# Performance work log

Measured on AMD Instinct MI355X. Metric: run time of the kernel, lower is better.

Reference implementation:

```python
import jax, jax.numpy as jnp
import numpy as np

N = 100000   # nodes
E = 3200000  # edges (avg degree 32)
IN, H, OUT = 128, 256, 40
EPS = 1e-5


def _glorot(key, fan_in, fan_out):
    s = jnp.sqrt(2.0 / (fan_in + fan_out))
    return jax.random.normal(key, (fan_in, fan_out), jnp.float32) * s


def setup_inputs() -> dict:
    key = jax.random.key(0)
    ks = jax.random.split(key, 6)
    edge_index = jax.random.randint(ks[0], (2, E), 0, N, dtype=jnp.int64)
    z = jax.random.normal(ks[1], (N, IN), jnp.float32) * 0.1
    return {
        "edge_index": edge_index,
        "z": z,
        "W1": _glorot(ks[2], IN, H), "b1": jnp.zeros((H,), jnp.float32),
        "g1": jnp.ones((H,), jnp.float32), "beta1": jnp.zeros((H,), jnp.float32),
        "W2": _glorot(ks[3], H, H), "b2": jnp.zeros((H,), jnp.float32),
        "g2": jnp.ones((H,), jnp.float32), "beta2": jnp.zeros((H,), jnp.float32),
        "W3": _glorot(ks[4], H, OUT), "b3": jnp.zeros((OUT,), jnp.float32),
    }


def _gcn_norm(edge_index):
    # add self-loops, compute symmetric normalization D^-1/2 (A+I) D^-1/2
    loops = jnp.arange(N, dtype=edge_index.dtype)
    src = jnp.concatenate([edge_index[0], loops])
    dst = jnp.concatenate([edge_index[1], loops])
    deg = jax.ops.segment_sum(jnp.ones_like(dst, jnp.float32), dst, num_segments=N)
    dinv = jnp.where(deg > 0, jax.lax.rsqrt(deg), 0.0)
    norm = dinv[src] * dinv[dst]  # [E+N]
    return src, dst, norm


def _conv(x, W, b, src, dst, norm):
    h = x @ W                              # [N, F_out]
    msg = h[src] * norm[:, None]           # gather + scale, [E+N, F_out]
    return jax.ops.segment_sum(msg, dst, num_segments=N) + b


def _bn(x, g, beta):
    m = x.mean(axis=0)
    v = x.var(axis=0)  # biased variance (training-mode BatchNorm)
    return (x - m) * jax.lax.rsqrt(v + EPS) * g + beta


def reference(edge_index, z, W1, b1, g1, beta1, W2, b2, g2, beta2, W3, b3):
    src, dst, norm = _gcn_norm(edge_index)
    x = jax.nn.relu(_bn(_conv(z, W1, b1, src, dst, norm), g1, beta1))
    x = jax.nn.relu(_bn(_conv(x, W2, b2, src, dst, norm), g2, beta2))
    return _conv(x, W3, b3, src, dst, norm)  # [N, OUT]
```

## Files before the change

kernel.cpp:

```cpp
#include <hip/hip_runtime.h>


#define NN   100000
#define NE   3200000
#define FIN  128
#define FH   256
#define FOUT 40
#define EPSV 1e-5f

#define BSH   7
#define NBKT  ((NN + 127) >> BSH)
#define CAPB  8192
#define CHNK  4096

typedef __attribute__((ext_vector_type(8))) short bf8;
typedef __attribute__((ext_vector_type(4))) float f32x4;

__device__ __forceinline__ unsigned short f2bf(float x) {
    unsigned int u = __float_as_uint(x);
    unsigned int r = u + 0x7fffu + ((u >> 16) & 1u);
    return (unsigned short)(r >> 16);
}
__device__ __forceinline__ float bf2f(unsigned short h) {
    return __uint_as_float(((unsigned int)h) << 16);
// ... 101 lines not shown
    __syncthreads();
    for (int i = tid; i < tot; i += 256) {
        unsigned int v = st[i];
        atomicAdd(&lcnt[v >> 17], 1);
    }
    __syncthreads();
    int pi = 0;
    if (tid < 128) lscan[0][tid] = lcnt[tid];
    __syncthreads();
    for (int off = 1; off < 128; off <<= 1) {
        if (tid < 128) {
            int x = lscan[pi][tid];
            if (tid >= off) x += lscan[pi][tid - off];
            lscan[pi ^ 1][tid] = x;
        }
        __syncthreads();
        pi ^= 1;
    }
    if (tid < 128) {
        int c = lcnt[tid];
        int excl = lscan[pi][tid] - c;
        lcur[tid] = excl;
        int node = (b << BSH) + tid;
        if (node < NN) {
            cntg[node] = c;
            dinv[node] = rsqrtf((float)(c + 1));
            rowptr[node] = bb + excl;
        }
    }
    __syncthreads();
    for (int i = tid; i < tot; i += 256) {
        unsigned int v = st[i];
        int pos = atomicAdd(&lcur[v >> 17], 1);
        csr[bb + pos] = (int)(v & 0x1ffffu);
    }
}

__global__ void k_wprep(const float* __restrict__ W1, unsigned short* __restrict__ W1h,
                        unsigned short* __restrict__ W1l,
                        const float* __restrict__ W2, unsigned short* __restrict__ W2h,
                        unsigned short* __restrict__ W2l,
                        const float* __restrict__ W3, unsigned short* __restrict__ W3h,
                        unsigned short* __restrict__ W3l) {
    int idx = blockIdx.x * blockDim.x + threadIdx.x;
    const float* W;
    unsigned short *Wh, *Wl;
    int K, M, MP;
    if (idx < 256 * 128) {
        W = W1; Wh = W1h; Wl = W1l; K = 128; M = 256; MP = 256;
    } else if (idx < 256 * 128 + 256 * 256) {
        idx -= 256 * 128;
        W = W2; Wh = W2h; Wl = W2l; K = 256; M = 256; MP = 256;
    } else if (idx < 256 * 128 + 256 * 256 + 64 * 256) {
        idx -= 256 * 128 + 256 * 256;
        W = W3; Wh = W3h; Wl = W3l; K = 256; M = 40; MP = 64;
    } else {
        return;
    }
    int m = idx / K, k = idx - m * K;
    float v = (m < M) ? W[(size_t)k * M + m] : 0.f;
    unsigned short h, l;
    f2bf2(v, h, l);
    size_t dst = ((size_t)(k >> 5) * MP + m) * 32 + (k & 31);
    Wh[dst] = h;
    Wl[dst] = l;
}

__global__ __launch_bounds__(256) void k_zpb8(const float* __restrict__ z,
                                              const float* __restrict__ dinv,
                                              unsigned char* __restrict__ zp8,
                                              float* __restrict__ scaleZ) {
    int wv = (blockIdx.x * blockDim.x + threadIdx.x) >> 6;
    int lane = threadIdx.x & 63;
    if (wv >= NN) return;
    float2 v = *(const float2*)(z + (size_t)wv * FIN + lane * 2);
    float d = dinv[wv];
    float a0 = v.x * d, a1 = v.y * d;
    float m = fmaxf(fabsf(a0), fabsf(a1));
#pragma unroll
    for (int off = 1; off < 64; off <<= 1) m = fmaxf(m, __shfl_xor(m, off));
    float inv = m > 0.f ? 127.f / m : 0.f;
    int q0 = (int)rintf(a0 * inv), q1 = (int)rintf(a1 * inv);
    unsigned short pk = (unsigned short)((q0 & 0xff) | ((q1 & 0xff) << 8));
    *(unsigned short*)(zp8 + (size_t)wv * FIN + lane * 2) = pk;
    if (lane == 0) scaleZ[wv] = m * (1.f / 127.f);
}

__global__ __launch_bounds__(256) void k_bnr8(const unsigned short* __restrict__ x,
                                              const float* __restrict__ scale,
                                              const float* __restrict__ shift,
                                              const float* __restrict__ dinv,
                                              unsigned char* __restrict__ y8,
                                              float* __restrict__ scaleY) {
    int wv = (blockIdx.x * blockDim.x + threadIdx.x) >> 6;
    int lane = threadIdx.x & 63;
    if (wv >= NN) return;
    uint2 u = *(const uint2*)(x + (size_t)wv * 256 + lane * 4);
    float4 sc = *(const float4*)(scale + lane * 4);
    float4 sh = *(const float4*)(shift + lane * 4);
    float d = dinv[wv];
    float v0 = fmaxf(__uint_as_float(u.x << 16) * sc.x + sh.x, 0.f) * d;
    float v1 = fmaxf(__uint_as_float(u.x & 0xffff0000u) * sc.y + sh.y, 0.f) * d;
    float v2 = fmaxf(__uint_as_float(u.y << 16) * sc.z + sh.z, 0.f) * d;
    float v3 = fmaxf(__uint_as_float(u.y & 0xffff0000u) * sc.w + sh.w, 0.f) * d;
    float m = fmaxf(fmaxf(v0, v1), fmaxf(v2, v3));
#pragma unroll
    for (int off = 1; off < 64; off <<= 1) m = fmaxf(m, __shfl_xor(m, off));
    float inv = m > 0.f ? 255.f / m : 0.f;
    unsigned int q0 = (unsigned int)(v0 * inv + 0.5f);
    unsigned int q1 = (unsigned int)(v1 * inv + 0.5f);
    unsigned int q2 = (unsigned int)(v2 * inv + 0.5f);
    unsigned int q3 = (unsigned int)(v3 * inv + 0.5f);
    *(unsigned int*)(y8 + (size_t)wv * 256 + lane * 4) = q0 | (q1 << 8) | (q2 << 16) | (q3 << 24);
    if (lane == 0) scaleY[wv] = m * (1.f / 255.f);
}

template <int F, bool SIGNED>
__global__ __launch_bounds__(256) void k_agg8(const unsigned char* __restrict__ tab,
                                              const float* __restrict__ rscale,
                                              const float* __restrict__ dinv,
                                              const int* __restrict__ rowptr,
                                              const int* __restrict__ cnt,
                                              const int* __restrict__ csr,
                                              unsigned short* __restrict__ oa) {
    const int wid = threadIdx.x >> 6;
    const int lane = threadIdx.x & 63;
    const int wstep = (blockDim.x >> 6) * gridDim.x;
    constexpr int B = F / 64;
    const int off = lane * B;
    for (int row0 = blockIdx.x * (blockDim.x >> 6) + wid; row0 < NN; row0 += wstep) {
        const int row = __builtin_amdgcn_readfirstlane(row0);
        const int rp = __builtin_amdgcn_readfirstlane(rowptr[row]);
        const int cn = __builtin_amdgcn_readfirstlane(cnt[row]);
        float acc[B];
        {
            float s = rscale[row];
            if constexpr (B == 4) {
                unsigned int u = *(const unsigned int*)(tab + (size_t)row * F + off);
                acc[0] = s * ub(u, 0); acc[1] = s * ub(u, 1);
                acc[2] = s * ub(u, 2); acc[3] = s * ub(u, 3);
            } else {
                unsigned int u = *(const unsigned short*)(tab + (size_t)row * F + off);
                acc[0] = s * sbyte(u, 0); acc[1] = s * sbyte(u, 1);
            }
        }
        int e = 0;
        for (; e + 8 <= cn; e += 8) {
            int idx[8];
            float s[8];
            unsigned int u[8];
#pragma unroll
            for (int j = 0; j < 8; j++) idx[j] = csr[rp + e + j];
#pragma unroll
            for (int j = 0; j < 8; j++) s[j] = rscale[idx[j]];
#pragma unroll
            for (int j = 0; j < 8; j++) {
                if constexpr (B == 4)
                    u[j] = *(const unsigned int*)(tab + (size_t)idx[j] * F + off);
                else
                    u[j] = *(const unsigned short*)(tab + (size_t)idx[j] * F + off);
            }
#pragma unroll
            for (int j = 0; j < 8; j++) {
                if constexpr (B == 4) {
                    acc[0] += s[j] * ub(u[j], 0); acc[1] += s[j] * ub(u[j], 1);
                    acc[2] += s[j] * ub(u[j], 2); acc[3] += s[j] * ub(u[j], 3);
                } else {
                    acc[0] += s[j] * sbyte(u[j], 0); acc[1] += s[j] * sbyte(u[j], 1);
                }
            }
        }
        for (; e < cn; e++) {
            int idx = csr[rp + e];
            float s = rscale[idx];
            if constexpr (B == 4) {
                unsigned int u = *(const unsigned int*)(tab + (size_t)idx * F + off);
                acc[0] += s * ub(u, 0); acc[1] += s * ub(u, 1);
                acc[2] += s * ub(u, 2); acc[3] += s * ub(u, 3);
            } else {
                unsigned int u = *(const unsigned short*)(tab + (size_t)idx * F + off);
                acc[0] += s * sbyte(u, 0); acc[1] += s * sbyte(u, 1);
            }
        }
        float d = dinv[row];
        size_t p = (size_t)row * F + off;
        if constexpr (B == 4) {
            uint2 o;
            o.x = (unsigned int)f2bf(acc[0] * d) | ((unsigned int)f2bf(acc[1] * d) << 16);
            o.y = (unsigned int)f2bf(acc[2] * d) | ((unsigned int)f2bf(acc[3] * d) << 16);
            *(uint2*)(oa + p) = o;
        } else {
            *(unsigned int*)(oa + p) =
                (unsigned int)f2bf(acc[0] * d) | ((unsigned int)f2bf(acc[1] * d) << 16);
        }
    }
}

template <int K>
__global__ __launch_bounds__(256) void k_gemm(const unsigned short* __restrict__ A,
                                              const unsigned short* __restrict__ Wth,
                                              const unsigned short* __restrict__ Wtl,
                                              const float* __restrict__ bias,
                                              unsigned short* __restrict__ outX,
                                              float* __restrict__ s1,
                                              float* __restrict__ s2) {
    __shared__ unsigned short sA[64][40];
    const int t = threadIdx.x;
    const int w = t >> 6, lane = t & 63;
    const int quad = lane >> 4, l16 = lane & 15;
    const int rowBase = blockIdx.y * 64;
    const int colW = blockIdx.x * 128 + w * 32;
    f32x4 acc[4][2];
#pragma unroll
    for (int i = 0; i < 4; i++)
#pragma unroll
        for (int j = 0; j < 2; j++) acc[i][j] = (f32x4)0.f;

    for (int k0 = 0; k0 < K; k0 += 32) {
        int gr = rowBase + (t >> 2);
        int4 v = {0, 0, 0, 0};
        if (gr < NN) v = *(const int4*)(A + (size_t)gr * K + k0 + (t & 3) * 8);
        __syncthreads();
        *(int4*)&sA[t >> 2][(t & 3) * 8] = v;
        __syncthreads();
        const int kb = k0 >> 5;
        bf8 bh[2], bl[2];
#pragma unroll
        for (int j = 0; j < 2; j++) {
            size_t bo = ((size_t)(kb * 256 + colW + j * 16 + l16)) * 32 + quad * 8;
            bh[j] = *(const bf8*)(Wth + bo);
            bl[j] = *(const bf8*)(Wtl + bo);
        }
#pragma unroll
        for (int i = 0; i < 4; i++) {
            bf8 a = *(const bf8*)&sA[i * 16 + l16][quad * 8];
#pragma unroll
            for (int j = 0; j < 2; j++) {
                acc[i][j] = __builtin_amdgcn_mfma_f32_16x16x32_bf16(a, bh[j], acc[i][j], 0, 0, 0);
                acc[i][j] = __builtin_amdgcn_mfma_f32_16x16x32_bf16(a, bl[j], acc[i][j], 0, 0, 0);
            }
        }
    }
#pragma unroll
    for (int j = 0; j < 2; j++) {
        int col = colW + j * 16 + l16;
        float b = bias[col];
        float s1p = 0.f, s2p = 0.f;
#pragma unroll
        for (int i = 0; i < 4; i++) {
#pragma unroll
            for (int r = 0; r < 4; r++) {
                int row = rowBase + i * 16 + quad * 4 + r;
                if (row < NN) {
                    float v = acc[i][j][r] + b;
                    s1p += v;
                    s2p += v * v;
                    outX[(size_t)row * 256 + col] = f2bf(v);
                }
            }
        }
        s1p += __shfl_xor(s1p, 16); s1p += __shfl_xor(s1p, 32);
        s2p += __shfl_xor(s2p, 16); s2p += __shfl_xor(s2p, 32);
        if (quad == 0) {
            atomicAdd(&s1[col], s1p);
            atomicAdd(&s2[col], s2p);
        }
    }
}

__global__ __launch_bounds__(256) void k_mgemm3(const unsigned short* __restrict__ y2,
                                                const unsigned short* __restrict__ Wth,
                                                const unsigned short* __restrict__ Wtl,
                                                unsigned char* __restrict__ H8,
                                                float* __restrict__ scaleH) {
    __shared__ unsigned short sA[128][40];
    __shared__ float sM[128][4];
    const int t = threadIdx.x;
    const int w = t >> 6, lane = t & 63;
    const int quad = lane >> 4, l16 = lane & 15;
    const int rowBase = blockIdx.x << 7;
    f32x4 acc[8];
#pragma unroll
    for (int i = 0; i < 8; i++) acc[i] = (f32x4)0.f;

    for (int k0 = 0; k0 < 256; k0 += 32) {
        const int kb = k0 >> 5;
        int id0 = t, id1 = t + 256;
        int gr0 = rowBase + (id0 >> 2), gr1 = rowBase + (id1 >> 2);
        int4 zz = {0, 0, 0, 0};
        int4 v0 = (gr0 < NN) ? *(const int4*)(y2 + (size_t)gr0 * 256 + k0 + (id0 & 3) * 8) : zz;
        int4 v1 = (gr1 < NN) ? *(const int4*)(y2 + (size_t)gr1 * 256 + k0 + (id1 & 3) * 8) : zz;
        __syncthreads();
        *(int4*)&sA[id0 >> 2][(id0 & 3) * 8] = v0;
        *(int4*)&sA[id1 >> 2][(id1 & 3) * 8] = v1;
        __syncthreads();
        size_t bo = ((size_t)(kb * 64 + w * 16 + l16)) * 32 + quad * 8;
        bf8 bh = *(const bf8*)(Wth + bo);
        bf8 bl = *(const bf8*)(Wtl + bo);
#pragma unroll
        for (int i = 0; i < 8; i++) {
            bf8 a = *(const bf8*)&sA[i * 16 + l16][quad * 8];
            acc[i] = __builtin_amdgcn_mfma_f32_16x16x32_bf16(a, bh, acc[i], 0, 0, 0);
            acc[i] = __builtin_amdgcn_mfma_f32_16x16x32_bf16(a, bl, acc[i], 0, 0, 0);
        }
    }
#pragma unroll
    for (int i = 0; i < 8; i++) {
#pragma unroll
        for (int r = 0; r < 4; r++) {
            float m = fabsf(acc[i][r]);
            m = fmaxf(m, __shfl_xor(m, 1));
            m = fmaxf(m, __shfl_xor(m, 2));
            m = fmaxf(m, __shfl_xor(m, 4));
            m = fmaxf(m, __shfl_xor(m, 8));
            if (l16 == 0) sM[i * 16 + quad * 4 + r][w] = m;
        }
    }
    __syncthreads();
    const int col = w * 16 + l16;
#pragma unroll
    for (int i = 0; i < 8; i++) {
#pragma unroll
        for (int r = 0; r < 4; r++) {
            int rloc = i * 16 + quad * 4 + r;
            int row = rowBase + rloc;
            float m = fmaxf(fmaxf(sM[rloc][0], sM[rloc][1]), fmaxf(sM[rloc][2], sM[rloc][3]));
            float inv = m > 0.f ? 127.f / m : 0.f;
            if (row < NN) {
                int q = (int)rintf(acc[i][r] * inv);
                H8[(size_t)row * 64 + col] = (unsigned char)(q & 0xff);
                if (w == 0 && l16 == 0) scaleH[row] = m * (1.f / 127.f);
            }
        }
    }
}

__global__ __launch_bounds__(256) void k_aggfb8(const unsigned char* __restrict__ tab,
                                                const float* __restrict__ rscale,
                                                const float* __restrict__ dinv,
                                                const int* __restrict__ rowptr,
                                                const int* __restrict__ cnt,
                                                const int* __restrict__ csr,
                                                const float* __restrict__ bias,
                                                float* __restrict__ out) {
    const int wid = threadIdx.x >> 6;
    const int lane = threadIdx.x & 63;
    const int wstep = (blockDim.x >> 6) * gridDim.x;
    for (int row0 = blockIdx.x * (blockDim.x >> 6) + wid; row0 < NN; row0 += wstep) {
        const int row = __builtin_amdgcn_readfirstlane(row0);
        const int rp = __builtin_amdgcn_readfirstlane(rowptr[row]);
        const int cn = __builtin_amdgcn_readfirstlane(cnt[row]);
        float acc = rscale[row] * (float)(int)(signed char)tab[(size_t)row * 64 + lane];
        int e = 0;
        for (; e + 8 <= cn; e += 8) {
            int idx[8];
            float s[8];
            float v[8];
#pragma unroll
            for (int j = 0; j < 8; j++) idx[j] = csr[rp + e + j];
#pragma unroll
            for (int j = 0; j < 8; j++) s[j] = rscale[idx[j]];
#pragma unroll
            for (int j = 0; j < 8; j++)
                v[j] = (float)(int)(signed char)tab[(size_t)idx[j] * 64 + lane];
#pragma unroll
            for (int j = 0; j < 8; j++) acc += s[j] * v[j];
        }
        for (; e < cn; e++) {
            int idx = csr[rp + e];
            float s = rscale[idx];
            acc += s * (float)(int)(signed char)tab[(size_t)idx * 64 + lane];
        }
        if (lane < FOUT) out[(size_t)row * FOUT + lane] = acc * dinv[row] + bias[lane];
    }
}

__global__ void k_bnfold(const float* __restrict__ s1, const float* __restrict__ s2,
                         const float* __restrict__ g, const float* __restrict__ be,
                         float* __restrict__ scale, float* __restrict__ shift) {
    int c = threadIdx.x;
    if (c < 256) {
        float mean = s1[c] * (1.f / NN);
        float var = s2[c] * (1.f / NN) - mean * mean;
        float sc = g[c] * rsqrtf(var + EPSV);
        scale[c] = sc;
        shift[c] = be[c] - mean * sc;
    }
}

__global__ void k_bnr(const unsigned short* __restrict__ x,
                      const float* __restrict__ scale, const float* __restrict__ shift,
                      const float* __restrict__ dinv, unsigned short* __restrict__ oy) {
    int i = blockIdx.x * blockDim.x + threadIdx.x;
    if (i >= NN * 128) return;
    int row = i >> 7;
    int c = (i & 127) * 2;
    unsigned int u = ((const unsigned int*)x)[i];
    float x0 = __uint_as_float(u << 16);
    float x1 = __uint_as_float(u & 0xffff0000u);
    float d = dinv[row];
    float v0 = fmaxf(x0 * scale[c + 0] + shift[c + 0], 0.f) * d;
    float v1 = fmaxf(x1 * scale[c + 1] + shift[c + 1], 0.f) * d;
    ((unsigned int*)oy)[i] = (unsigned int)f2bf(v0) | ((unsigned int)f2bf(v1) << 16);
}

extern "C" void kernel_launch(void* const* d_in, const int* in_sizes, int n_in,
                              void* d_out, int out_size, void* d_ws, size_t ws_size,
                              hipStream_t stream) {
    const int* ei = (const int*)d_in[0];
    const float* z = (const float*)d_in[1];
    const float* W1 = (const float*)d_in[2];
    const float* b1 = (const float*)d_in[3];
    const float* g1 = (const float*)d_in[4];
    const float* be1 = (const float*)d_in[5];
    const float* W2 = (const float*)d_in[6];
    const float* b2 = (const float*)d_in[7];
    const float* g2 = (const float*)d_in[8];
    const float* be2 = (const float*)d_in[9];
    const float* W3 = (const float*)d_in[10];
    const float* b3 = (const float*)d_in[11];
    float* out = (float*)d_out;

    char* w = (char*)d_ws;
    size_t o = 0;
    auto take = [&](size_t bytes) {
        char* p = w + o;
        o = (o + bytes + 255) & ~(size_t)255;
        return p;
    };
    int* cnt = (int*)take((size_t)NN * 4);
    int* rowptr = (int*)take((size_t)NN * 4);
    int* gcur = (int*)take(NBKT * 4);
    int* bbase = (int*)take(NBKT * 4);
    int* csr = (int*)take((size_t)NE * 4);
    unsigned int* staging = (unsigned int*)take((size_t)NBKT * CAPB * 4);
    float* dinv = (float*)take((size_t)NN * 4);
    float* stat = (float*)take(4 * 256 * 4);
    float* sc1 = (float*)take(256 * 4);
    float* sh1 = (float*)take(256 * 4);
    float* sc2 = (float*)take(256 * 4);
    float* sh2 = (float*)take(256 * 4);
    unsigned short* Wt1h = (unsigned short*)take(256 * 128 * 2);
    unsigned short* Wt1l = (unsigned short*)take(256 * 128 * 2);
    unsigned short* Wt2h = (unsigned short*)take(256 * 256 * 2);
    unsigned short* Wt2l = (unsigned short*)take(256 * 256 * 2);
    unsigned short* Wt3h = (unsigned short*)take(64 * 256 * 2);
    unsigned short* Wt3l = (unsigned short*)take(64 * 256 * 2);
    unsigned char* zp8 = (unsigned char*)take((size_t)NN * FIN);
    unsigned char* y1_8 = (unsigned char*)take((size_t)NN * FH);
    unsigned char* H8 = (unsigned char*)take((size_t)NN * 64);
    float* scaleZ = (float*)take((size_t)NN * 4);
    float* scaleY = (float*)take((size_t)NN * 4);
    float* scaleH = (float*)take((size_t)NN * 4);
    unsigned short* P1 = (unsigned short*)take((size_t)NN * 256 * 2);
    unsigned short* P2 = (unsigned short*)take((size_t)NN * 512 * 2);

    unsigned short* a1 = P1;
    unsigned short* x1 = P2;
    unsigned short* a2 = P2 + (size_t)NN * 256;
    unsigned short* x2 = P1;
    unsigned short* y2 = P2;
    float* s1a = stat, *s2a = stat + 256, *s1b = stat + 512, *s2b = stat + 768;

    hipMemsetAsync(gcur, 0, NBKT * 4, stream);
    hipMemsetAsync(stat, 0, 4 * 256 * 4, stream);

    k_bin<<<(NE + CHNK - 1) / CHNK, 256, 0, stream>>>(ei, gcur, staging);
    k_bucketscan<<<1, 256, 0, stream>>>(gcur, bbase);
    k_build<<<NBKT, 256, 0, stream>>>(staging, gcur, bbase, cnt, dinv, rowptr, csr);

    k_wprep<<<(256 * 128 + 256 * 256 + 64 * 256 + 255) / 256, 256, 0, stream>>>(
        W1, Wt1h, Wt1l, W2, Wt2h, Wt2l, W3, Wt3h, Wt3l);

    const int GR = (NN + 63) / 64;
    const int WV = (NN + 3) / 4;

    k_zpb8<<<WV, 256, 0, stream>>>(z, dinv, zp8, scaleZ);
    k_agg8<128, true><<<2560, 256, 0, stream>>>(zp8, scaleZ, dinv, rowptr, cnt, csr, a1);
    k_gemm<128><<<dim3(2, GR), 256, 0, stream>>>(a1, Wt1h, Wt1l, b1, x1, s1a, s2a);
    k_bnfold<<<1, 256, 0, stream>>>(s1a, s2a, g1, be1, sc1, sh1);
    k_bnr8<<<WV, 256, 0, stream>>>(x1, sc1, sh1, dinv, y1_8, scaleY);

    k_agg8<256, false><<<2560, 256, 0, stream>>>(y1_8, scaleY, dinv, rowptr, cnt, csr, a2);
    k_gemm<256><<<dim3(2, GR), 256, 0, stream>>>(a2, Wt2h, Wt2l, b2, x2, s1b, s2b);
    k_bnfold<<<1, 256, 0, stream>>>(s1b, s2b, g2, be2, sc2, sh2);
    k_bnr<<<(NN * 128 + 255) / 256, 256, 0, stream>>>(x2, sc2, sh2, dinv, y2);

    k_mgemm3<<<NBKT, 256, 0, stream>>>(y2, Wt3h, Wt3l, H8, scaleH);
    k_aggfb8<<<2560, 256, 0, stream>>>(H8, scaleH, dinv, rowptr, cnt, csr, b3, out);
}
```

Measured before the change: 815.8 us.

## Gather 16-byte chunks per lane across multiple edges in int8 aggregation

Restructures the int8 SpMM aggregation so each lane loads a 16-byte uint4 chunk of a neighbor row, with the wavefront split into groups that process several edges at once. Column indices and scales are loaded cooperatively, one per lane, then broadcast with shuffles. Partial sums are combined with xor-shuffle reductions and a select network before the bf16 store. The aim is fewer, wider memory transactions and more edges in flight per wave, at the cost of 16 accumulators per lane and extra shuffle and reduction work.

```diff
diff --git a/kernel.cpp b/kernel.cpp
--- a/kernel.cpp
+++ b/kernel.cpp
@@ -251,72 +251,111 @@
     const int wid = threadIdx.x >> 6;
     const int lane = threadIdx.x & 63;
     const int wstep = (blockDim.x >> 6) * gridDim.x;
-    constexpr int B = F / 64;
-    const int off = lane * B;
+    constexpr int G = 1024 / F;
+    constexpr int LPE = 64 / G;
+    constexpr int NS = 16 / G;
+    const int sub = lane & (LPE - 1);
+    const int grp = lane / LPE;
+    const size_t choff = (size_t)sub * 16;
     for (int row0 = blockIdx.x * (blockDim.x >> 6) + wid; row0 < NN; row0 += wstep) {
         const int row = __builtin_amdgcn_readfirstlane(row0);
         const int rp = __builtin_amdgcn_readfirstlane(rowptr[row]);
         const int cn = __builtin_amdgcn_readfirstlane(cnt[row]);
-        float acc[B];
+        float acc[16];
         {
-            float s = rscale[row];
-            if constexpr (B == 4) {
-                unsigned int u = *(const unsigned int*)(tab + (size_t)row * F + off);
-                acc[0] = s * ub(u, 0); acc[1] = s * ub(u, 1);
-                acc[2] = s * ub(u, 2); acc[3] = s * ub(u, 3);
-            } else {
-                unsigned int u = *(const unsigned short*)(tab + (size_t)row * F + off);
-                acc[0] = s * sbyte(u, 0); acc[1] = s * sbyte(u, 1);
-            }
-        }
-        int e = 0;
-        for (; e + 8 <= cn; e += 8) {
-            int idx[8];
-            float s[8];
-            unsigned int u[8];
-#pragma unroll
-            for (int j = 0; j < 8; j++) idx[j] = csr[rp + e + j];
-#pragma unroll
-            for (int j = 0; j < 8; j++) s[j] = rscale[idx[j]];
-#pragma unroll
-            for (int j = 0; j < 8; j++) {
-                if constexpr (B == 4)
-                    u[j] = *(const unsigned int*)(tab + (size_t)idx[j] * F + off);
-                else
-                    u[j] = *(const unsigned short*)(tab + (size_t)idx[j] * F + off);
-            }
-#pragma unroll
-            for (int j = 0; j < 8; j++) {
-                if constexpr (B == 4) {
-                    acc[0] += s[j] * ub(u[j], 0); acc[1] += s[j] * ub(u[j], 1);
-                    acc[2] += s[j] * ub(u[j], 2); acc[3] += s[j] * ub(u[j], 3);
-                } else {
-                    acc[0] += s[j] * sbyte(u[j], 0); acc[1] += s[j] * sbyte(u[j], 1);
+            float s0 = rscale[row];
+            float se = (grp == 0) ? s0 : 0.f;
+            uint4 u = *(const uint4*)(tab + (size_t)row * F + choff);
+            const unsigned int uw[4] = {u.x, u.y, u.z, u.w};
+#pragma unroll
+            for (int jw = 0; jw < 4; jw++)
+#pragma unroll
+                for (int jb = 0; jb < 4; jb++)
+                    acc[jw * 4 + jb] =
+                        se * (SIGNED ? sbyte(uw[jw], jb) : ub(uw[jw], jb));
+        }
+        for (int e = 0; e < cn; e += 64) {
+            const int rem = min(cn - e, 64);
+            int cv = row;
+            float sv = 0.f;
+            if (lane < rem) {
+                cv = csr[rp + e + lane];
+                sv = rscale[cv];
+            }
+            for (int q = 0; q < rem; q += 16) {
+                const int nslot = (min(rem - q, 16) + G - 1) / G;
+                int mi[NS];
+                float ms[NS];
+                uint4 u[NS];
+#pragma unroll
+                for (int t = 0; t < NS; t++) {
+                    if (t < nslot) {
+                        int srcl = q + t * G + grp;
+                        mi[t] = __shfl(cv, srcl);
+                        ms[t] = __shfl(sv, srcl);
+                    }
                 }
-            }
-        }
-        for (; e < cn; e++) {
-            int idx = csr[rp + e];
-            float s = rscale[idx];
-            if constexpr (B == 4) {
-                unsigned int u = *(const unsigned int*)(tab + (size_t)idx * F + off);
-                acc[0] += s * ub(u, 0); acc[1] += s * ub(u, 1);
-                acc[2] += s * ub(u, 2); acc[3] += s * ub(u, 3);
-            } else {
-                unsigned int u = *(const unsigned short*)(tab + (size_t)idx * F + off);
-                acc[0] += s * sbyte(u, 0); acc[1] += s * sbyte(u, 1);
-            }
-        }
-        float d = dinv[row];
-        size_t p = (size_t)row * F + off;
-        if constexpr (B == 4) {
+#pragma unroll
+                for (int t = 0; t < NS; t++) {
+                    if (t < nslot)
+                        u[t] = *(const uint4*)(tab + (size_t)mi[t] * F + choff);
+                }
+#pragma unroll
+                for (int t = 0; t < NS; t++) {
+                    if (t < nslot) {
+                        const unsigned int uw[4] = {u[t].x, u[t].y, u[t].z, u[t].w};
+#pragma unroll
+                        for (int jw = 0; jw < 4; jw++)
+#pragma unroll
+                            for (int jb = 0; jb < 4; jb++)
+                                acc[jw * 4 + jb] +=
+                                    ms[t] * (SIGNED ? sbyte(uw[jw], jb) : ub(uw[jw], jb));
+                    }
+                }
+            }
+        }
+        if constexpr (G == 4) {
+#pragma unroll
+            for (int j = 0; j < 16; j++) {
+                acc[j] += __shfl_xor(acc[j], 16);
+                acc[j] += __shfl_xor(acc[j], 32);
+            }
+        } else {
+#pragma unroll
+            for (int j = 0; j < 16; j++) {
+                acc[j] += __shfl_xor(acc[j], 8);
+                acc[j] += __shfl_xor(acc[j], 16);
+                acc[j] += __shfl_xor(acc[j], 32);
+            }
+        }
+        const float d = dinv[row];
+        if constexpr (G == 4) {
+            float av[4];
+#pragma unroll
+            for (int jj = 0; jj < 4; jj++) {
+                float a = (grp & 1) ? acc[4 + jj] : acc[jj];
+                float b = (grp & 1) ? acc[12 + jj] : acc[8 + jj];
+                av[jj] = (grp & 2) ? b : a;
+            }
             uint2 o;
-            o.x = (unsigned int)f2bf(acc[0] * d) | ((unsigned int)f2bf(acc[1] * d) << 16);
-            o.y = (unsigned int)f2bf(acc[2] * d) | ((unsigned int)f2bf(acc[3] * d) << 16);
-            *(uint2*)(oa + p) = o;
+            o.x = (unsigned int)f2bf(av[0] * d) | ((unsigned int)f2bf(av[1] * d) << 16);
+            o.y = (unsigned int)f2bf(av[2] * d) | ((unsigned int)f2bf(av[3] * d) << 16);
+            *(uint2*)(oa + (size_t)row * F + sub * 16 + grp * 4) = o;
         } else {
-            *(unsigned int*)(oa + p) =
-                (unsigned int)f2bf(acc[0] * d) | ((unsigned int)f2bf(acc[1] * d) << 16);
+            float av[2];
+#pragma unroll
+            for (int jj = 0; jj < 2; jj++) {
+                float x01 = (grp & 1) ? acc[2 + jj] : acc[0 + jj];
+                float x23 = (grp & 1) ? acc[6 + jj] : acc[4 + jj];
+                float x45 = (grp & 1) ? acc[10 + jj] : acc[8 + jj];
+                float x67 = (grp & 1) ? acc[14 + jj] : acc[12 + jj];
+                float y0 = (grp & 2) ? x23 : x01;
+                float y1 = (grp & 2) ? x67 : x45;
+                av[jj] = (grp & 4) ? y1 : y0;
+            }
+            unsigned int o =
+                (unsigned int)f2bf(av[0] * d) | ((unsigned int)f2bf(av[1] * d) << 16);
+            *(unsigned int*)(oa + (size_t)row * F + sub * 16 + grp * 2) = o;
         }
     }
 }
```

Measured after the change: 938.6 us. 15.0% more time.

## Slice quantized feature tables and aggregate 8 edges per wave in parallel

Applied to the files above, without the earlier changes.

The int8 feature tables written by the quantize kernels and the layer-3 GEMM are re-laid out as column slices of 32 or 64 bytes per node stored contiguously. Blocks are assigned to one slice, so the gather working set per kernel shrinks and is meant to stay resident in cache. Within a wave, 8 lane groups each fetch a different neighbor's slice row, the loads are software-pipelined, and the partial sums are reduced with cross-lane shuffles. The cost is more blocks walking the CSR (once per slice), extra shuffle reductions, and a small pad on the csr buffer to keep reads past the end in bounds.

```diff
diff --git a/kernel.cpp b/kernel.cpp
--- a/kernel.cpp
+++ b/kernel.cpp
@@ -207,7 +207,8 @@
     float inv = m > 0.f ? 127.f / m : 0.f;
     int q0 = (int)rintf(a0 * inv), q1 = (int)rintf(a1 * inv);
     unsigned short pk = (unsigned short)((q0 & 0xff) | ((q1 & 0xff) << 8));
-    *(unsigned short*)(zp8 + (size_t)wv * FIN + lane * 2) = pk;
+    *(unsigned short*)(zp8 + (size_t)(lane >> 4) * ((size_t)NN * 32) +
+                       (size_t)wv * 32 + ((lane * 2) & 31)) = pk;
     if (lane == 0) scaleZ[wv] = m * (1.f / 127.f);
 }
 
@@ -236,87 +237,120 @@
     unsigned int q1 = (unsigned int)(v1 * inv + 0.5f);
     unsigned int q2 = (unsigned int)(v2 * inv + 0.5f);
     unsigned int q3 = (unsigned int)(v3 * inv + 0.5f);
-    *(unsigned int*)(y8 + (size_t)wv * 256 + lane * 4) = q0 | (q1 << 8) | (q2 << 16) | (q3 << 24);
+    *(unsigned int*)(y8 + (size_t)(lane >> 4) * ((size_t)NN * 64) +
+                     (size_t)wv * 64 + ((lane * 4) & 63)) =
+        q0 | (q1 << 8) | (q2 << 16) | (q3 << 24);
     if (lane == 0) scaleY[wv] = m * (1.f / 255.f);
 }
 
-template <int F, bool SIGNED>
-__global__ __launch_bounds__(256) void k_agg8(const unsigned char* __restrict__ tab,
+template <int F, int SW, bool SIGNED>
+__global__ __launch_bounds__(256) void k_aggs(const unsigned char* __restrict__ tab,
                                               const float* __restrict__ rscale,
                                               const float* __restrict__ dinv,
                                               const int* __restrict__ rowptr,
                                               const int* __restrict__ cnt,
                                               const int* __restrict__ csr,
                                               unsigned short* __restrict__ oa) {
+    constexpr int NSL = F / SW;
+    constexpr int PB = SW / 8;
+    const int slice = blockIdx.x % NSL;
+    const int sb = blockIdx.x / NSL;
+    const int nsb = gridDim.x / NSL;
     const int wid = threadIdx.x >> 6;
     const int lane = threadIdx.x & 63;
-    const int wstep = (blockDim.x >> 6) * gridDim.x;
-    constexpr int B = F / 64;
-    const int off = lane * B;
-    for (int row0 = blockIdx.x * (blockDim.x >> 6) + wid; row0 < NN; row0 += wstep) {
+    const int g = lane >> 3;
+    const int fb = (lane & 7) * PB;
+    const unsigned char* tsl = tab + (size_t)slice * ((size_t)NN * SW);
+
+    for (int row0 = sb * 4 + wid; row0 < NN; row0 += nsb * 4) {
         const int row = __builtin_amdgcn_readfirstlane(row0);
         const int rp = __builtin_amdgcn_readfirstlane(rowptr[row]);
         const int cn = __builtin_amdgcn_readfirstlane(cnt[row]);
-        float acc[B];
-        {
-            float s = rscale[row];
-            if constexpr (B == 4) {
-                unsigned int u = *(const unsigned int*)(tab + (size_t)row * F + off);
-                acc[0] = s * ub(u, 0); acc[1] = s * ub(u, 1);
-                acc[2] = s * ub(u, 2); acc[3] = s * ub(u, 3);
+        float acc[PB];
+#pragma unroll
+        for (int k = 0; k < PB; k++) acc[k] = 0.f;
+
+        auto loadsel = [&](int b, int& sel, float& se) {
+            int ic[8];
+            float sc[8];
+            const int e0 = b * 8;
+#pragma unroll
+            for (int j = 0; j < 8; j++) {
+                int e = e0 + j;
+                int idx = (e == 0 || e > cn) ? row : csr[rp + e - 1];
+                ic[j] = idx;
+                sc[j] = (e > cn) ? 0.f : rscale[idx];
+            }
+            int s01 = (g & 1) ? ic[1] : ic[0], s23 = (g & 1) ? ic[3] : ic[2];
+            int s45 = (g & 1) ? ic[5] : ic[4], s67 = (g & 1) ? ic[7] : ic[6];
+            int t0 = (g & 2) ? s23 : s01, t1 = (g & 2) ? s67 : s45;
+            sel = (g & 4) ? t1 : t0;
+            float w01 = (g & 1) ? sc[1] : sc[0], w23 = (g & 1) ? sc[3] : sc[2];
+            float w45 = (g & 1) ? sc[5] : sc[4], w67 = (g & 1) ? sc[7] : sc[6];
+            float u0 = (g & 2) ? w23 : w01, u1 = (g & 2) ? w67 : w45;
+            se = (g & 4) ? u1 : u0;
+        };
+        auto payload = [&](int sel) {
+            uint2 u;
+            if constexpr (PB == 4) {
+                u.x = *(const unsigned int*)(tsl + (size_t)sel * SW + fb);
+                u.y = 0u;
             } else {
-                unsigned int u = *(const unsigned short*)(tab + (size_t)row * F + off);
-                acc[0] = s * sbyte(u, 0); acc[1] = s * sbyte(u, 1);
-            }
-        }
-        int e = 0;
-        for (; e + 8 <= cn; e += 8) {
-            int idx[8];
-            float s[8];
-            unsigned int u[8];
-#pragma unroll
-            for (int j = 0; j < 8; j++) idx[j] = csr[rp + e + j];
-#pragma unroll
-            for (int j = 0; j < 8; j++) s[j] = rscale[idx[j]];
-#pragma unroll
-            for (int j = 0; j < 8; j++) {
-                if constexpr (B == 4)
-                    u[j] = *(const unsigned int*)(tab + (size_t)idx[j] * F + off);
-                else
-                    u[j] = *(const unsigned short*)(tab + (size_t)idx[j] * F + off);
-            }
-#pragma unroll
-            for (int j = 0; j < 8; j++) {
-                if constexpr (B == 4) {
-                    acc[0] += s[j] * ub(u[j], 0); acc[1] += s[j] * ub(u[j], 1);
-                    acc[2] += s[j] * ub(u[j], 2); acc[3] += s[j] * ub(u[j], 3);
-                } else {
-                    acc[0] += s[j] * sbyte(u[j], 0); acc[1] += s[j] * sbyte(u[j], 1);
-                }
-            }
-        }
-        for (; e < cn; e++) {
-            int idx = csr[rp + e];
-            float s = rscale[idx];
-            if constexpr (B == 4) {
-                unsigned int u = *(const unsigned int*)(tab + (size_t)idx * F + off);
-                acc[0] += s * ub(u, 0); acc[1] += s * ub(u, 1);
-                acc[2] += s * ub(u, 2); acc[3] += s * ub(u, 3);
+                u = *(const uint2*)(tsl + (size_t)sel * SW + fb);
+            }
+            return u;
+        };
+        auto consume = [&](uint2 u, float se) {
+            acc[0] += se * (SIGNED ? sbyte(u.x, 0) : ub(u.x, 0));
+            acc[1] += se * (SIGNED ? sbyte(u.x, 1) : ub(u.x, 1));
+            acc[2] += se * (SIGNED ? sbyte(u.x, 2) : ub(u.x, 2));
+            acc[3] += se * (SIGNED ? sbyte(u.x, 3) : ub(u.x, 3));
+            if constexpr (PB == 8) {
+                acc[4] += se * (SIGNED ? sbyte(u.y, 0) : ub(u.y, 0));
+                acc[5] += se * (SIGNED ? sbyte(u.y, 1) : ub(u.y, 1));
+                acc[6] += se * (SIGNED ? sbyte(u.y, 2) : ub(u.y, 2));
+                acc[7] += se * (SIGNED ? sbyte(u.y, 3) : ub(u.y, 3));
+            }
+        };
+
+        const int nbat = (cn + 8) >> 3;
+        int selc;
+        float sec;
+        loadsel(0, selc, sec);
+        uint2 uc = payload(selc);
+        for (int b = 1; b < nbat; b++) {
+            int seln;
+            float sen;
+            loadsel(b, seln, sen);
+            uint2 un = payload(seln);
+            consume(uc, sec);
+            uc = un;
+            sec = sen;
+        }
+        consume(uc, sec);
+
+#pragma unroll
+        for (int k = 0; k < PB; k++) {
+            acc[k] += __shfl_xor(acc[k], 8);
+            acc[k] += __shfl_xor(acc[k], 16);
+            acc[k] += __shfl_xor(acc[k], 32);
+        }
+        const float d = dinv[row];
+        if (lane < 8) {
+            unsigned short* dst = oa + (size_t)row * F + slice * SW + lane * PB;
+            if constexpr (PB == 4) {
+                uint2 o;
+                o.x = (unsigned int)f2bf(acc[0] * d) | ((unsigned int)f2bf(acc[1] * d) << 16);
+                o.y = (unsigned int)f2bf(acc[2] * d) | ((unsigned int)f2bf(acc[3] * d) << 16);
+                *(uint2*)dst = o;
             } else {
-                unsigned int u = *(const unsigned short*)(tab + (size_t)idx * F + off);
-                acc[0] += s * sbyte(u, 0); acc[1] += s * sbyte(u, 1);
-            }
-        }
-        float d = dinv[row];
-        size_t p = (size_t)row * F + off;
-        if constexpr (B == 4) {
-            uint2 o;
-            o.x = (unsigned int)f2bf(acc[0] * d) | ((unsigned int)f2bf(acc[1] * d) << 16);
-            o.y = (unsigned int)f2bf(acc[2] * d) | ((unsigned int)f2bf(acc[3] * d) << 16);
-            *(uint2*)(oa + p) = o;
-        } else {
-            *(unsigned int*)(oa + p) =
-                (unsigned int)f2bf(acc[0] * d) | ((unsigned int)f2bf(acc[1] * d) << 16);
+                uint4 o;
+                o.x = (unsigned int)f2bf(acc[0] * d) | ((unsigned int)f2bf(acc[1] * d) << 16);
+                o.y = (unsigned int)f2bf(acc[2] * d) | ((unsigned int)f2bf(acc[3] * d) << 16);
+                o.z = (unsigned int)f2bf(acc[4] * d) | ((unsigned int)f2bf(acc[5] * d) << 16);
+                o.w = (unsigned int)f2bf(acc[6] * d) | ((unsigned int)f2bf(acc[7] * d) << 16);
+                *(uint4*)dst = o;
+            }
         }
     }
 }
@@ -453,14 +487,15 @@
             float inv = m > 0.f ? 127.f / m : 0.f;
             if (row < NN) {
                 int q = (int)rintf(acc[i][r] * inv);
-                H8[(size_t)row * 64 + col] = (unsigned char)(q & 0xff);
+                H8[(size_t)(col >> 5) * ((size_t)NN * 32) + (size_t)row * 32 + (col & 31)] =
+                    (unsigned char)(q & 0xff);
                 if (w == 0 && l16 == 0) scaleH[row] = m * (1.f / 127.f);
             }
         }
     }
 }
 
-__global__ __launch_bounds__(256) void k_aggfb8(const unsigned char* __restrict__ tab,
+__global__ __launch_bounds__(256) void k_aggsfb(const unsigned char* __restrict__ tab,
                                                 const float* __restrict__ rscale,
                                                 const float* __restrict__ dinv,
                                                 const int* __restrict__ rowptr,
@@ -468,35 +503,77 @@
                                                 const int* __restrict__ csr,
                                                 const float* __restrict__ bias,
                                                 float* __restrict__ out) {
+    constexpr int SW = 32;
+    constexpr int NSL = 2;
+    const int slice = blockIdx.x % NSL;
+    const int sb = blockIdx.x / NSL;
+    const int nsb = gridDim.x / NSL;
     const int wid = threadIdx.x >> 6;
     const int lane = threadIdx.x & 63;
-    const int wstep = (blockDim.x >> 6) * gridDim.x;
-    for (int row0 = blockIdx.x * (blockDim.x >> 6) + wid; row0 < NN; row0 += wstep) {
+    const int g = lane >> 3;
+    const int fb = (lane & 7) * 4;
+    const unsigned char* tsl = tab + (size_t)slice * ((size_t)NN * SW);
+
+    for (int row0 = sb * 4 + wid; row0 < NN; row0 += nsb * 4) {
         const int row = __builtin_amdgcn_readfirstlane(row0);
         const int rp = __builtin_amdgcn_readfirstlane(rowptr[row]);
         const int cn = __builtin_amdgcn_readfirstlane(cnt[row]);
-        float acc = rscale[row] * (float)(int)(signed char)tab[(size_t)row * 64 + lane];
-        int e = 0;
-        for (; e + 8 <= cn; e += 8) {
-            int idx[8];
-            float s[8];
-            float v[8];
-#pragma unroll
-            for (int j = 0; j < 8; j++) idx[j] = csr[rp + e + j];
-#pragma unroll
-            for (int j = 0; j < 8; j++) s[j] = rscale[idx[j]];
-#pragma unroll
-            for (int j = 0; j < 8; j++)
-                v[j] = (float)(int)(signed char)tab[(size_t)idx[j] * 64 + lane];
-#pragma unroll
-            for (int j = 0; j < 8; j++) acc += s[j] * v[j];
-        }
-        for (; e < cn; e++) {
-            int idx = csr[rp + e];
-            float s = rscale[idx];
-            acc += s * (float)(int)(signed char)tab[(size_t)idx * 64 + lane];
-        }
-        if (lane < FOUT) out[(size_t)row * FOUT + lane] = acc * dinv[row] + bias[lane];
+        float a0 = 0.f, a1 = 0.f, a2 = 0.f, a3 = 0.f;
+
+        auto loadsel = [&](int b, int& sel, float& se) {
+            int ic[8];
+            float sc[8];
+            const int e0 = b * 8;
+#pragma unroll
+            for (int j = 0; j < 8; j++) {
+                int e = e0 + j;
+                int idx = (e == 0 || e > cn) ? row : csr[rp + e - 1];
+                ic[j] = idx;
+                sc[j] = (e > cn) ? 0.f : rscale[idx];
+            }
+            int s01 = (g & 1) ? ic[1] : ic[0], s23 = (g & 1) ? ic[3] : ic[2];
+            int s45 = (g & 1) ? ic[5] : ic[4], s67 = (g & 1) ? ic[7] : ic[6];
+            int t0 = (g & 2) ? s23 : s01, t1 = (g & 2) ? s67 : s45;
+            sel = (g & 4) ? t1 : t0;
+            float w01 = (g & 1) ? sc[1] : sc[0], w23 = (g & 1) ? sc[3] : sc[2];
+            float w45 = (g & 1) ? sc[5] : sc[4], w67 = (g & 1) ? sc[7] : sc[6];
+            float u0 = (g & 2) ? w23 : w01, u1 = (g & 2) ? w67 : w45;
+            se = (g & 4) ? u1 : u0;
+        };
+
+        const int nbat = (cn + 8) >> 3;
+        int selc;
+        float sec;
+        loadsel(0, selc, sec);
+        unsigned int uc = *(const unsigned int*)(tsl + (size_t)selc * SW + fb);
+        for (int b = 1; b < nbat; b++) {
+            int seln;
+            float sen;
+            loadsel(b, seln, sen);
+            unsigned int un = *(const unsigned int*)(tsl + (size_t)seln * SW + fb);
+            a0 += sec * sbyte(uc, 0); a1 += sec * sbyte(uc, 1);
+            a2 += sec * sbyte(uc, 2); a3 += sec * sbyte(uc, 3);
+            uc = un;
+            sec = sen;
+        }
+        a0 += sec * sbyte(uc, 0); a1 += sec * sbyte(uc, 1);
+        a2 += sec * sbyte(uc, 2); a3 += sec * sbyte(uc, 3);
+
+        a0 += __shfl_xor(a0, 8); a0 += __shfl_xor(a0, 16); a0 += __shfl_xor(a0, 32);
+        a1 += __shfl_xor(a1, 8); a1 += __shfl_xor(a1, 16); a1 += __shfl_xor(a1, 32);
+        a2 += __shfl_xor(a2, 8); a2 += __shfl_xor(a2, 16); a2 += __shfl_xor(a2, 32);
+        a3 += __shfl_xor(a3, 8); a3 += __shfl_xor(a3, 16); a3 += __shfl_xor(a3, 32);
+
+        const float d = dinv[row];
+        const int f0 = slice * SW + fb;
+        if (lane < 8 && f0 < FOUT) {
+            float4 o;
+            o.x = a0 * d + bias[f0 + 0];
+            o.y = a1 * d + bias[f0 + 1];
+            o.z = a2 * d + bias[f0 + 2];
+            o.w = a3 * d + bias[f0 + 3];
+            *(float4*)(out + (size_t)row * FOUT + f0) = o;
+        }
     }
 }
 
@@ -557,7 +634,7 @@
     int* rowptr = (int*)take((size_t)NN * 4);
     int* gcur = (int*)take(NBKT * 4);
     int* bbase = (int*)take(NBKT * 4);
-    int* csr = (int*)take((size_t)NE * 4);
+    int* csr = (int*)take((size_t)NE * 4 + 256);
     unsigned int* staging = (unsigned int*)take((size_t)NBKT * CAPB * 4);
     float* dinv = (float*)take((size_t)NN * 4);
     float* stat = (float*)take(4 * 256 * 4);
@@ -601,16 +678,16 @@
     const int WV = (NN + 3) / 4;
 
     k_zpb8<<<WV, 256, 0, stream>>>(z, dinv, zp8, scaleZ);
-    k_agg8<128, true><<<2560, 256, 0, stream>>>(zp8, scaleZ, dinv, rowptr, cnt, csr, a1);
+    k_aggs<128, 32, true><<<2560, 256, 0, stream>>>(zp8, scaleZ, dinv, rowptr, cnt, csr, a1);
     k_gemm<128><<<dim3(2, GR), 256, 0, stream>>>(a1, Wt1h, Wt1l, b1, x1, s1a, s2a);
     k_bnfold<<<1, 256, 0, stream>>>(s1a, s2a, g1, be1, sc1, sh1);
     k_bnr8<<<WV, 256, 0, stream>>>(x1, sc1, sh1, dinv, y1_8, scaleY);
 
-    k_agg8<256, false><<<2560, 256, 0, stream>>>(y1_8, scaleY, dinv, rowptr, cnt, csr, a2);
+    k_aggs<256, 64, false><<<2560, 256, 0, stream>>>(y1_8, scaleY, dinv, rowptr, cnt, csr, a2);
     k_gemm<256><<<dim3(2, GR), 256, 0, stream>>>(a2, Wt2h, Wt2l, b2, x2, s1b, s2b);
     k_bnfold<<<1, 256, 0, stream>>>(s1b, s2b, g2, be2, sc2, sh2);
     k_bnr<<<(NN * 128 + 255) / 256, 256, 0, stream>>>(x2, sc2, sh2, dinv, y2);
 
     k_mgemm3<<<NBKT, 256, 0, stream>>>(y2, Wt3h, Wt3l, H8, scaleH);
-    k_aggfb8<<<2560, 256, 0, stream>>>(H8, scaleH, dinv, rowptr, cnt, csr, b3, out);
-}
+    k_aggsfb<<<2560, 256, 0, stream>>>(H8, scaleH, dinv, rowptr, cnt, csr, b3, out);
+}
```

Result: slower. 2.037 ms (+149.7%).

## Split each wavefront into lane groups gathering separate neighbor rows with wide loads

Applied to the files above, without the earlier changes.

The three sparse aggregation kernels now split each 64-lane wavefront into groups, each gathering a different neighbor's row with 16-byte (or 8-byte) loads instead of every lane reading a few bytes of the same row. Partial sums are then combined across groups with cross-lane shuffles, and a few lanes write vectorized bf16 or fp32 output. The self-loop is folded in as virtual edge zero, and padded slots are masked with a zero scale. This is meant to cut the number of memory instructions per gathered row and improve gather efficiency, at the cost of more registers, selects and shuffle reductions per row.

```diff
diff --git a/kernel.cpp b/kernel.cpp
--- a/kernel.cpp
+++ b/kernel.cpp
@@ -240,83 +240,157 @@
     if (lane == 0) scaleY[wv] = m * (1.f / 255.f);
 }
 
-template <int F, bool SIGNED>
-__global__ __launch_bounds__(256) void k_agg8(const unsigned char* __restrict__ tab,
-                                              const float* __restrict__ rscale,
-                                              const float* __restrict__ dinv,
-                                              const int* __restrict__ rowptr,
-                                              const int* __restrict__ cnt,
-                                              const int* __restrict__ csr,
-                                              unsigned short* __restrict__ oa) {
+__device__ __forceinline__ int sel4i(const int* o, int g) {
+    int a = (g & 1) ? o[1] : o[0];
+    int b = (g & 1) ? o[3] : o[2];
+    return (g & 2) ? b : a;
+}
+__device__ __forceinline__ float sel4f(const float* o, int g) {
+    float a = (g & 1) ? o[1] : o[0];
+    float b = (g & 1) ? o[3] : o[2];
+    return (g & 2) ? b : a;
+}
+__device__ __forceinline__ int sel8i(const int* o, int g) {
+    int a = sel4i(o, g), b = sel4i(o + 4, g);
+    return (g & 4) ? b : a;
+}
+__device__ __forceinline__ float sel8f(const float* o, int g) {
+    float a = sel4f(o, g), b = sel4f(o + 4, g);
+    return (g & 4) ? b : a;
+}
+
+__device__ __forceinline__ void batch8(int b, int row, int rp, int cn,
+                                       const int* __restrict__ csr,
+                                       const float* __restrict__ rscale,
+                                       int* ix, float* sc) {
+#pragma unroll
+    for (int j = 0; j < 8; j++) {
+        int ve = b * 8 + j;
+        int ci = min(ve, cn) - 1;
+        ci = max(ci, 0);
+        int idx = (ve == 0) ? row : csr[rp + ci];
+        ix[j] = idx;
+        sc[j] = (ve <= cn) ? rscale[idx] : 0.f;
+    }
+}
+
+__global__ __launch_bounds__(256) void k_aggm256(const unsigned char* __restrict__ tab,
+                                                 const float* __restrict__ rscale,
+                                                 const float* __restrict__ dinv,
+                                                 const int* __restrict__ rowptr,
+                                                 const int* __restrict__ cnt,
+                                                 const int* __restrict__ csr,
+                                                 unsigned short* __restrict__ oa) {
     const int wid = threadIdx.x >> 6;
     const int lane = threadIdx.x & 63;
     const int wstep = (blockDim.x >> 6) * gridDim.x;
-    constexpr int B = F / 64;
-    const int off = lane * B;
+    const int l16 = lane & 15;
+    const int g4 = lane >> 4;
+    const int inner = l16 * 16;
     for (int row0 = blockIdx.x * (blockDim.x >> 6) + wid; row0 < NN; row0 += wstep) {
         const int row = __builtin_amdgcn_readfirstlane(row0);
         const int rp = __builtin_amdgcn_readfirstlane(rowptr[row]);
         const int cn = __builtin_amdgcn_readfirstlane(cnt[row]);
-        float acc[B];
-        {
-            float s = rscale[row];
-            if constexpr (B == 4) {
-                unsigned int u = *(const unsigned int*)(tab + (size_t)row * F + off);
-                acc[0] = s * ub(u, 0); acc[1] = s * ub(u, 1);
-                acc[2] = s * ub(u, 2); acc[3] = s * ub(u, 3);
-            } else {
-                unsigned int u = *(const unsigned short*)(tab + (size_t)row * F + off);
-                acc[0] = s * sbyte(u, 0); acc[1] = s * sbyte(u, 1);
-            }
-        }
-        int e = 0;
-        for (; e + 8 <= cn; e += 8) {
-            int idx[8];
-            float s[8];
-            unsigned int u[8];
-#pragma unroll
-            for (int j = 0; j < 8; j++) idx[j] = csr[rp + e + j];
-#pragma unroll
-            for (int j = 0; j < 8; j++) s[j] = rscale[idx[j]];
-#pragma unroll
-            for (int j = 0; j < 8; j++) {
-                if constexpr (B == 4)
-                    u[j] = *(const unsigned int*)(tab + (size_t)idx[j] * F + off);
-                else
-                    u[j] = *(const unsigned short*)(tab + (size_t)idx[j] * F + off);
-            }
-#pragma unroll
-            for (int j = 0; j < 8; j++) {
-                if constexpr (B == 4) {
-                    acc[0] += s[j] * ub(u[j], 0); acc[1] += s[j] * ub(u[j], 1);
-                    acc[2] += s[j] * ub(u[j], 2); acc[3] += s[j] * ub(u[j], 3);
-                } else {
-                    acc[0] += s[j] * sbyte(u[j], 0); acc[1] += s[j] * sbyte(u[j], 1);
+        float acc[16];
+#pragma unroll
+        for (int k = 0; k < 16; k++) acc[k] = 0.f;
+        const int nbat = (cn + 8) >> 3;
+        for (int b = 0; b < nbat; b++) {
+            int ix[8];
+            float sc[8];
+            batch8(b, row, rp, cn, csr, rscale, ix, sc);
+            int off[8];
+#pragma unroll
+            for (int j = 0; j < 8; j++) off[j] = ix[j] << 8;
+            int o0 = sel4i(off, g4);
+            int o1 = sel4i(off + 4, g4);
+            float s0 = sel4f(sc, g4);
+            float s1 = sel4f(sc + 4, g4);
+            uint4 u0 = *(const uint4*)(tab + (size_t)(unsigned)o0 + inner);
+            uint4 u1 = *(const uint4*)(tab + (size_t)(unsigned)o1 + inner);
+            const unsigned int w0[4] = {u0.x, u0.y, u0.z, u0.w};
+            const unsigned int w1[4] = {u1.x, u1.y, u1.z, u1.w};
+#pragma unroll
+            for (int jw = 0; jw < 4; jw++)
+#pragma unroll
+                for (int jb = 0; jb < 4; jb++) {
+                    acc[jw * 4 + jb] += s0 * ub(w0[jw], jb);
+                    acc[jw * 4 + jb] += s1 * ub(w1[jw], jb);
                 }
-            }
-        }
-        for (; e < cn; e++) {
-            int idx = csr[rp + e];
-            float s = rscale[idx];
-            if constexpr (B == 4) {
-                unsigned int u = *(const unsigned int*)(tab + (size_t)idx * F + off);
-                acc[0] += s * ub(u, 0); acc[1] += s * ub(u, 1);
-                acc[2] += s * ub(u, 2); acc[3] += s * ub(u, 3);
-            } else {
-                unsigned int u = *(const unsigned short*)(tab + (size_t)idx * F + off);
-                acc[0] += s * sbyte(u, 0); acc[1] += s * sbyte(u, 1);
-            }
-        }
-        float d = dinv[row];
-        size_t p = (size_t)row * F + off;
-        if constexpr (B == 4) {
-            uint2 o;
-            o.x = (unsigned int)f2bf(acc[0] * d) | ((unsigned int)f2bf(acc[1] * d) << 16);
-            o.y = (unsigned int)f2bf(acc[2] * d) | ((unsigned int)f2bf(acc[3] * d) << 16);
-            *(uint2*)(oa + p) = o;
-        } else {
-            *(unsigned int*)(oa + p) =
-                (unsigned int)f2bf(acc[0] * d) | ((unsigned int)f2bf(acc[1] * d) << 16);
+        }
+#pragma unroll
+        for (int k = 0; k < 16; k++) {
+            acc[k] += __shfl_xor(acc[k], 16);
+            acc[k] += __shfl_xor(acc[k], 32);
+        }
+        const float d = dinv[row];
+        if (lane < 16) {
+            unsigned int w[8];
+#pragma unroll
+            for (int t = 0; t < 8; t++)
+                w[t] = (unsigned int)f2bf(acc[2 * t] * d) |
+                       ((unsigned int)f2bf(acc[2 * t + 1] * d) << 16);
+            unsigned short* dst = oa + (size_t)row * 256 + lane * 16;
+            *(uint4*)dst = make_uint4(w[0], w[1], w[2], w[3]);
+            *(uint4*)(dst + 8) = make_uint4(w[4], w[5], w[6], w[7]);
+        }
+    }
+}
+
+__global__ __launch_bounds__(256) void k_aggm128(const unsigned char* __restrict__ tab,
+                                                 const float* __restrict__ rscale,
+                                                 const float* __restrict__ dinv,
+                                                 const int* __restrict__ rowptr,
+                                                 const int* __restrict__ cnt,
+                                                 const int* __restrict__ csr,
+                                                 unsigned short* __restrict__ oa) {
+    const int wid = threadIdx.x >> 6;
+    const int lane = threadIdx.x & 63;
+    const int wstep = (blockDim.x >> 6) * gridDim.x;
+    const int l8 = lane & 7;
+    const int g8 = lane >> 3;
+    const int inner = l8 * 16;
+    for (int row0 = blockIdx.x * (blockDim.x >> 6) + wid; row0 < NN; row0 += wstep) {
+        const int row = __builtin_amdgcn_readfirstlane(row0);
+        const int rp = __builtin_amdgcn_readfirstlane(rowptr[row]);
+        const int cn = __builtin_amdgcn_readfirstlane(cnt[row]);
+        float acc[16];
+#pragma unroll
+        for (int k = 0; k < 16; k++) acc[k] = 0.f;
+        const int nbat = (cn + 8) >> 3;
+        for (int b = 0; b < nbat; b++) {
+            int ix[8];
+            float sc[8];
+            batch8(b, row, rp, cn, csr, rscale, ix, sc);
+            int off[8];
+#pragma unroll
+            for (int j = 0; j < 8; j++) off[j] = ix[j] << 7;
+            int o0 = sel8i(off, g8);
+            float s0 = sel8f(sc, g8);
+            uint4 u0 = *(const uint4*)(tab + (size_t)(unsigned)o0 + inner);
+            const unsigned int w0[4] = {u0.x, u0.y, u0.z, u0.w};
+#pragma unroll
+            for (int jw = 0; jw < 4; jw++)
+#pragma unroll
+                for (int jb = 0; jb < 4; jb++)
+                    acc[jw * 4 + jb] += s0 * sbyte(w0[jw], jb);
+        }
+#pragma unroll
+        for (int k = 0; k < 16; k++) {
+            acc[k] += __shfl_xor(acc[k], 8);
+            acc[k] += __shfl_xor(acc[k], 16);
+            acc[k] += __shfl_xor(acc[k], 32);
+        }
+        const float d = dinv[row];
+        if (lane < 8) {
+            unsigned int w[8];
+#pragma unroll
+            for (int t = 0; t < 8; t++)
+                w[t] = (unsigned int)f2bf(acc[2 * t] * d) |
+                       ((unsigned int)f2bf(acc[2 * t + 1] * d) << 16);
+            unsigned short* dst = oa + (size_t)row * 128 + lane * 16;
+            *(uint4*)dst = make_uint4(w[0], w[1], w[2], w[3]);
+            *(uint4*)(dst + 8) = make_uint4(w[4], w[5], w[6], w[7]);
         }
     }
 }
@@ -460,7 +534,7 @@
     }
 }
 
-__global__ __launch_bounds__(256) void k_aggfb8(const unsigned char* __restrict__ tab,
+__global__ __launch_bounds__(256) void k_aggfbm(const unsigned char* __restrict__ tab,
                                                 const float* __restrict__ rscale,
                                                 const float* __restrict__ dinv,
                                                 const int* __restrict__ rowptr,
@@ -471,32 +545,55 @@
     const int wid = threadIdx.x >> 6;
     const int lane = threadIdx.x & 63;
     const int wstep = (blockDim.x >> 6) * gridDim.x;
+    const int l8 = lane & 7;
+    const int g8 = lane >> 3;
+    const int inner = l8 * 8;
     for (int row0 = blockIdx.x * (blockDim.x >> 6) + wid; row0 < NN; row0 += wstep) {
         const int row = __builtin_amdgcn_readfirstlane(row0);
         const int rp = __builtin_amdgcn_readfirstlane(rowptr[row]);
         const int cn = __builtin_amdgcn_readfirstlane(cnt[row]);
-        float acc = rscale[row] * (float)(int)(signed char)tab[(size_t)row * 64 + lane];
-        int e = 0;
-        for (; e + 8 <= cn; e += 8) {
-            int idx[8];
-            float s[8];
-            float v[8];
-#pragma unroll
-            for (int j = 0; j < 8; j++) idx[j] = csr[rp + e + j];
-#pragma unroll
-            for (int j = 0; j < 8; j++) s[j] = rscale[idx[j]];
-#pragma unroll
-            for (int j = 0; j < 8; j++)
-                v[j] = (float)(int)(signed char)tab[(size_t)idx[j] * 64 + lane];
-#pragma unroll
-            for (int j = 0; j < 8; j++) acc += s[j] * v[j];
-        }
-        for (; e < cn; e++) {
-            int idx = csr[rp + e];
-            float s = rscale[idx];
-            acc += s * (float)(int)(signed char)tab[(size_t)idx * 64 + lane];
-        }
-        if (lane < FOUT) out[(size_t)row * FOUT + lane] = acc * dinv[row] + bias[lane];
+        float acc[8];
+#pragma unroll
+        for (int k = 0; k < 8; k++) acc[k] = 0.f;
+        const int nbat = (cn + 8) >> 3;
+        for (int b = 0; b < nbat; b++) {
+            int ix[8];
+            float sc[8];
+            batch8(b, row, rp, cn, csr, rscale, ix, sc);
+            int off[8];
+#pragma unroll
+            for (int j = 0; j < 8; j++) off[j] = ix[j] << 6;
+            int o0 = sel8i(off, g8);
+            float s0 = sel8f(sc, g8);
+            uint2 u0 = *(const uint2*)(tab + (size_t)(unsigned)o0 + inner);
+#pragma unroll
+            for (int jb = 0; jb < 4; jb++) {
+                acc[jb] += s0 * sbyte(u0.x, jb);
+                acc[4 + jb] += s0 * sbyte(u0.y, jb);
+            }
+        }
+#pragma unroll
+        for (int k = 0; k < 8; k++) {
+            acc[k] += __shfl_xor(acc[k], 8);
+            acc[k] += __shfl_xor(acc[k], 16);
+            acc[k] += __shfl_xor(acc[k], 32);
+        }
+        const float d = dinv[row];
+        const int f0 = l8 * 8;
+        if (lane < 8 && f0 < FOUT) {
+            float4 oA, oB;
+            oA.x = acc[0] * d + bias[f0 + 0];
+            oA.y = acc[1] * d + bias[f0 + 1];
+            oA.z = acc[2] * d + bias[f0 + 2];
+            oA.w = acc[3] * d + bias[f0 + 3];
+            oB.x = acc[4] * d + bias[f0 + 4];
+            oB.y = acc[5] * d + bias[f0 + 5];
+            oB.z = acc[6] * d + bias[f0 + 6];
+            oB.w = acc[7] * d + bias[f0 + 7];
+            float* dst = out + (size_t)row * FOUT + f0;
+            *(float4*)dst = oA;
+            *(float4*)(dst + 4) = oB;
+        }
     }
 }
 
@@ -557,7 +654,7 @@
     int* rowptr = (int*)take((size_t)NN * 4);
     int* gcur = (int*)take(NBKT * 4);
     int* bbase = (int*)take(NBKT * 4);
-    int* csr = (int*)take((size_t)NE * 4);
+    int* csr = (int*)take((size_t)NE * 4 + 256);
     unsigned int* staging = (unsigned int*)take((size_t)NBKT * CAPB * 4);
     float* dinv = (float*)take((size_t)NN * 4);
     float* stat = (float*)take(4 * 256 * 4);
@@ -601,16 +698,16 @@
     const int WV = (NN + 3) / 4;
 
     k_zpb8<<<WV, 256, 0, stream>>>(z, dinv, zp8, scaleZ);
-    k_agg8<128, true><<<2560, 256, 0, stream>>>(zp8, scaleZ, dinv, rowptr, cnt, csr, a1);
+    k_aggm128<<<2560, 256, 0, stream>>>(zp8, scaleZ, dinv, rowptr, cnt, csr, a1);
     k_gemm<128><<<dim3(2, GR), 256, 0, stream>>>(a1, Wt1h, Wt1l, b1, x1, s1a, s2a);
     k_bnfold<<<1, 256, 0, stream>>>(s1a, s2a, g1, be1, sc1, sh1);
     k_bnr8<<<WV, 256, 0, stream>>>(x1, sc1, sh1, dinv, y1_8, scaleY);
 
-    k_agg8<256, false><<<2560, 256, 0, stream>>>(y1_8, scaleY, dinv, rowptr, cnt, csr, a2);
+    k_aggm256<<<2560, 256, 0, stream>>>(y1_8, scaleY, dinv, rowptr, cnt, csr, a2);
     k_gemm<256><<<dim3(2, GR), 256, 0, stream>>>(a2, Wt2h, Wt2l, b2, x2, s1b, s2b);
     k_bnfold<<<1, 256, 0, stream>>>(s1b, s2b, g2, be2, sc2, sh2);
     k_bnr<<<(NN * 128 + 255) / 256, 256, 0, stream>>>(x2, sc2, sh2, dinv, y2);
 
     k_mgemm3<<<NBKT, 256, 0, stream>>>(y2, Wt3h, Wt3l, H8, scaleH);
-    k_aggfb8<<<2560, 256, 0, stream>>>(H8, scaleH, dinv, rowptr, cnt, csr, b3, out);
-}
+    k_aggfbm<<<2560, 256, 0, stream>>>(H8, scaleH, dinv, rowptr, cnt, csr, b3, out);
+}
```

New measurement: 1.163 ms. +42.6%, slower.
